# Performance work log

Hardware: AMD Instinct MI355X
Metric: run time of the kernel (lower is better)

## Reference

```python
import jax, jax.numpy as jnp
import numpy as np

TAU = 2.0      # LIF membrane time constant
VTH = 1.0      # firing threshold
ALPHA = 4.0    # sigmoid surrogate sharpness (spikingjelly default)
EPS = 1e-5     # BatchNorm eps


@jax.custom_vjp
def spike(x):
    # Heaviside forward, sigmoid surrogate backward
    return (x >= 0.0).astype(x.dtype)

def _spike_fwd(x):
    return (x >= 0.0).astype(x.dtype), x

def _spike_bwd(x, g):
    s = jax.nn.sigmoid(ALPHA * x)
    return (g * ALPHA * s * (1.0 - s),)

spike.defvjp(_spike_fwd, _spike_bwd)


def setup_inputs() -> dict:
    key = jax.random.key(0)
    k1, k2 = jax.random.split(key)
    T, B, C_in, C_out, M = 8, 16, 256, 256, 1024
    x = jax.random.normal(k1, (T, B, C_in, M), dtype=jnp.float32)
    W = jax.random.normal(k2, (C_out, C_in), dtype=jnp.float32) * 0.05  # 1x1 conv weight
    gamma = jnp.ones((C_out,), dtype=jnp.float32)
    beta = jnp.zeros((C_out,), dtype=jnp.float32)
    return {"x": x, "W": W, "gamma": gamma, "beta": beta}


def reference(x, W, gamma, beta):
    # 1x1 Conv1d over flattened (T*B) batch == channel contraction
    y = jnp.einsum('oc,tbcm->tbom', W, x)  # [T,B,C_out,M]
    # BatchNorm1d (training forward): per-channel stats over (T*B, M)
    mean = y.mean(axis=(0, 1, 3), keepdims=True)
    var = y.var(axis=(0, 1, 3), keepdims=True)
    y = (y - mean) * jax.lax.rsqrt(var + EPS)
    y = y * gamma[None, None, :, None] + beta[None, None, :, None]

    # Multi-step LIF: v <- v + (x - v)/tau; fire; hard reset to 0 (detached)
    def step(v, xt):
        v = v + (xt - v) / TAU
        s = spike(v - VTH)
        v = v * (1.0 - jax.lax.stop_gradient(s))
        return v, s

    v0 = jnp.zeros_like(y[0])
    _, spikes = jax.lax.scan(step, v0, y)
    return spikes  # [T,B,C_out,M]
```

## Files before the change

kernel.cpp:

```cpp
#include <hip/hip_runtime.h>

#define TT 8
#define BB 16
#define CC 256
#define MM 1024
#define NY 33554432


__device__ __forceinline__ float np_pairwise_1024(
    const float* __restrict__ yrow, float* __restrict__ scratch, int tid)
{
    if (tid < 64) {
        const int blk = tid >> 3;
        const int k   = tid & 7;
        const float* p = yrow + blk * 128 + k;
        float r = p[0];
#pragma unroll
        for (int i = 1; i < 16; ++i) r = __fadd_rn(r, p[8 * i]);
        scratch[tid] = r;
    }
    __syncthreads();
    if (tid == 0) {
        float B[8];
#pragma unroll
        for (int blk = 0; blk < 8; ++blk) {
            const float* r = scratch + blk * 8;
            const float s01 = __fadd_rn(r[0], r[1]);
            const float s23 = __fadd_rn(r[2], r[3]);
            const float s45 = __fadd_rn(r[4], r[5]);
            const float s67 = __fadd_rn(r[6], r[7]);
            B[blk] = __fadd_rn(__fadd_rn(s01, s23), __fadd_rn(s45, s67));
        }
        const float c0 = __fadd_rn(B[0], B[1]);
        const float c1 = __fadd_rn(B[2], B[3]);
        const float c2 = __fadd_rn(B[4], B[5]);
        const float c3 = __fadd_rn(B[6], B[7]);
        scratch[64] = __fadd_rn(__fadd_rn(c0, c1), __fadd_rn(c2, c3));
    }
    __syncthreads();
    return scratch[64];
}

__global__ __launch_bounds__(256) void einsum_store(
    const float* __restrict__ x, const float* __restrict__ W,
    float* __restrict__ y)
{
    __shared__ float wt[CC][8];
    const int tid = threadIdx.x;
    const int lin = blockIdx.x;
    const int xcd = lin & 7;
    const int j   = lin >> 3;
    const int og  = j & 31;
    const int tb  = xcd * 16 + (j >> 5);
    const int m0  = tid * 4;

#pragma unroll
    for (int i = 0; i < 8; ++i)
        wt[tid][i] = W[(size_t)(og * 8 + i) * CC + tid];
    __syncthreads();

    const float* xs = x + (size_t)tb * (CC * MM) + m0;

    float a[8][4];
#pragma unroll
    for (int i = 0; i < 8; ++i)
#pragma unroll
        for (int q = 0; q < 4; ++q) a[i][q] = 0.0f;

    for (int c = 0; c < CC; ++c) {
        const float4 xv = *(const float4*)(xs + (size_t)c * MM);
        const float4 w0 = *(const float4*)&wt[c][0];
        const float4 w1 = *(const float4*)&wt[c][4];
        const float wv[8] = {w0.x, w0.y, w0.z, w0.w, w1.x, w1.y, w1.z, w1.w};
#pragma unroll
        for (int i = 0; i < 8; ++i) {
            a[i][0] = __fadd_rn(a[i][0], __fmul_rn(wv[i], xv.x));
            a[i][1] = __fadd_rn(a[i][1], __fmul_rn(wv[i], xv.y));
            a[i][2] = __fadd_rn(a[i][2], __fmul_rn(wv[i], xv.z));
            a[i][3] = __fadd_rn(a[i][3], __fmul_rn(wv[i], xv.w));
        }
    }

#pragma unroll
    for (int i = 0; i < 8; ++i) {
        const int o = og * 8 + i;
        *(float4*)(y + ((size_t)tb * CC + o) * MM + m0) =
            make_float4(a[i][0], a[i][1], a[i][2], a[i][3]);
    }
}

__global__ __launch_bounds__(256) void mean_partial_y(
    const float* __restrict__ y, float* __restrict__ part)
{
    __shared__ float yrow[1024];
    __shared__ float scratch[65];
    const int tid = threadIdx.x;
    const int o  = blockIdx.x;
    const int tb = blockIdx.y;
    const int m0 = tid * 4;

    *(float4*)&yrow[m0] = *(const float4*)(y + ((size_t)tb * CC + o) * MM + m0);
    __syncthreads();
    const float P = np_pairwise_1024(yrow, scratch, tid);
    if (tid == 0) part[(size_t)tb * 256 + o] = P;
}

__global__ void reduce_mean(const float* __restrict__ part,
                            float* __restrict__ mv)
{
    const int o = threadIdx.x;
    float S = 0.0f;
    for (int tb = 0; tb < 128; ++tb)
        S = __fadd_rn(S, part[(size_t)tb * 256 + o]);
    mv[o] = S * (1.0f / 131072.0f);
}

__global__ __launch_bounds__(256) void var_partial_y(
    const float* __restrict__ y, const float* __restrict__ mv,
    float* __restrict__ part)
{
    __shared__ float yrow[1024];
    __shared__ float scratch[65];
    const int tid = threadIdx.x;
    const int o  = blockIdx.x;
    const int tb = blockIdx.y;
    const int m0 = tid * 4;

    const float mean = mv[o];
    const float4 yv = *(const float4*)(y + ((size_t)tb * CC + o) * MM + m0);
    const float d0 = __fsub_rn(yv.x, mean);
    const float d1 = __fsub_rn(yv.y, mean);
    const float d2 = __fsub_rn(yv.z, mean);
    const float d3 = __fsub_rn(yv.w, mean);
    *(float4*)&yrow[m0] = make_float4(__fmul_rn(d0, d0), __fmul_rn(d1, d1),
                                      __fmul_rn(d2, d2), __fmul_rn(d3, d3));
    __syncthreads();
    const float P = np_pairwise_1024(yrow, scratch, tid);
    if (tid == 0) part[(size_t)tb * 256 + o] = P;
}

__global__ void reduce_var(const float* __restrict__ part,
                           float* __restrict__ mv)
{
    const int o = threadIdx.x;
    float S = 0.0f;
    for (int tb = 0; tb < 128; ++tb)
        S = __fadd_rn(S, part[(size_t)tb * 256 + o]);
    const float var = S * (1.0f / 131072.0f);
    const float vp  = __fadd_rn(var, 1e-5f);
    mv[256 + o] = __fdiv_rn(1.0f, __fsqrt_rn(vp));
}

__global__ __launch_bounds__(256) void lif_from_y(
    const float* __restrict__ y, const float* __restrict__ mv,
    const float* __restrict__ gamma, const float* __restrict__ beta,
    float* __restrict__ out)
{
    const int tid = threadIdx.x;
    const int o = blockIdx.x;
    const int b = blockIdx.y;
    const int m0 = tid * 4;

    const float mean = mv[o];
    const float rs   = mv[256 + o];
    const float g    = gamma[o];
    const float be   = beta[o];

    float v0 = 0.0f, v1 = 0.0f, v2 = 0.0f, v3 = 0.0f;

    for (int t = 0; t < TT; ++t) {
        const size_t off = ((size_t)(t * BB + b) * CC + o) * MM + m0;
        const float4 yv = *(const float4*)(y + off);

        const float n0 = __fadd_rn(__fmul_rn(__fmul_rn(__fsub_rn(yv.x, mean), rs), g), be);
        const float n1 = __fadd_rn(__fmul_rn(__fmul_rn(__fsub_rn(yv.y, mean), rs), g), be);
        const float n2 = __fadd_rn(__fmul_rn(__fmul_rn(__fsub_rn(yv.z, mean), rs), g), be);
        const float n3 = __fadd_rn(__fmul_rn(__fmul_rn(__fsub_rn(yv.w, mean), rs), g), be);

        v0 = __fadd_rn(v0, __fmul_rn(__fsub_rn(n0, v0), 0.5f));
        v1 = __fadd_rn(v1, __fmul_rn(__fsub_rn(n1, v1), 0.5f));
        v2 = __fadd_rn(v2, __fmul_rn(__fsub_rn(n2, v2), 0.5f));
        v3 = __fadd_rn(v3, __fmul_rn(__fsub_rn(n3, v3), 0.5f));

        const bool s0 = (v0 >= 1.0f);
        const bool s1 = (v1 >= 1.0f);
        const bool s2 = (v2 >= 1.0f);
        const bool s3 = (v3 >= 1.0f);
        if (s0) v0 = 0.0f;
        if (s1) v1 = 0.0f;
        if (s2) v2 = 0.0f;
        if (s3) v3 = 0.0f;

        *(float4*)(out + off) = make_float4(s0 ? 1.0f : 0.0f, s1 ? 1.0f : 0.0f,
                                            s2 ? 1.0f : 0.0f, s3 ? 1.0f : 0.0f);
    }
}

__device__ __forceinline__ void e1_row4(
    const float* __restrict__ x, const float* __restrict__ W,
    int t, int b, int o, int m0,
    float& y0, float& y1, float& y2, float& y3)
{
    const float* xs = x + ((size_t)(t * BB + b) * CC) * MM + m0;
    const float* wr = W + (size_t)o * CC;
    y0 = 0.0f; y1 = 0.0f; y2 = 0.0f; y3 = 0.0f;
    for (int c = 0; c < CC; ++c) {
        const float wc = wr[c];
        const float4 xv = *(const float4*)(xs + (size_t)c * MM);
        y0 = __fadd_rn(y0, __fmul_rn(wc, xv.x));
        y1 = __fadd_rn(y1, __fmul_rn(wc, xv.y));
        y2 = __fadd_rn(y2, __fmul_rn(wc, xv.z));
        y3 = __fadd_rn(y3, __fmul_rn(wc, xv.w));
    }
}

__global__ __launch_bounds__(256) void pass_mean_fb(
    const float* __restrict__ x, const float* __restrict__ W,
    float* __restrict__ part)
{
    __shared__ float yrow[1024];
    __shared__ float scratch[65];
    const int tid = threadIdx.x;
    const int o  = blockIdx.x;
    const int tb = blockIdx.y;
    const int m0 = tid * 4;
    float y0, y1, y2, y3;
    e1_row4(x, W, tb >> 4, tb & 15, o, m0, y0, y1, y2, y3);
    *(float4*)&yrow[m0] = make_float4(y0, y1, y2, y3);
    __syncthreads();
    const float P = np_pairwise_1024(yrow, scratch, tid);
    if (tid == 0) part[(size_t)tb * 256 + o] = P;
}

__global__ __launch_bounds__(256) void pass_var_fb(
    const float* __restrict__ x, const float* __restrict__ W,
    const float* __restrict__ mv, float* __restrict__ part)
{
    __shared__ float yrow[1024];
    __shared__ float scratch[65];
    const int tid = threadIdx.x;
    const int o  = blockIdx.x;
    const int tb = blockIdx.y;
    const int m0 = tid * 4;
    const float mean = mv[o];
    float y0, y1, y2, y3;
    e1_row4(x, W, tb >> 4, tb & 15, o, m0, y0, y1, y2, y3);
    const float d0 = __fsub_rn(y0, mean);
    const float d1 = __fsub_rn(y1, mean);
    const float d2 = __fsub_rn(y2, mean);
    const float d3 = __fsub_rn(y3, mean);
    *(float4*)&yrow[m0] = make_float4(__fmul_rn(d0, d0), __fmul_rn(d1, d1),
                                      __fmul_rn(d2, d2), __fmul_rn(d3, d3));
    __syncthreads();
    const float P = np_pairwise_1024(yrow, scratch, tid);
    if (tid == 0) part[(size_t)tb * 256 + o] = P;
}

__global__ __launch_bounds__(256) void pass_lif_fb(
    const float* __restrict__ x, const float* __restrict__ W,
    const float* __restrict__ mv,
    const float* __restrict__ gamma, const float* __restrict__ beta,
    float* __restrict__ out)
{
    const int tid = threadIdx.x;
    const int o = blockIdx.x;
    const int b = blockIdx.y;
    const int m0 = tid * 4;
    const float mean = mv[o];
    const float rs   = mv[256 + o];
    const float g    = gamma[o];
    const float be   = beta[o];
    float v0 = 0.0f, v1 = 0.0f, v2 = 0.0f, v3 = 0.0f;
    for (int t = 0; t < TT; ++t) {
        float y0, y1, y2, y3;
        e1_row4(x, W, t, b, o, m0, y0, y1, y2, y3);
        const float n0 = __fadd_rn(__fmul_rn(__fmul_rn(__fsub_rn(y0, mean), rs), g), be);
        const float n1 = __fadd_rn(__fmul_rn(__fmul_rn(__fsub_rn(y1, mean), rs), g), be);
        const float n2 = __fadd_rn(__fmul_rn(__fmul_rn(__fsub_rn(y2, mean), rs), g), be);
        const float n3 = __fadd_rn(__fmul_rn(__fmul_rn(__fsub_rn(y3, mean), rs), g), be);
        v0 = __fadd_rn(v0, __fmul_rn(__fsub_rn(n0, v0), 0.5f));
        v1 = __fadd_rn(v1, __fmul_rn(__fsub_rn(n1, v1), 0.5f));
        v2 = __fadd_rn(v2, __fmul_rn(__fsub_rn(n2, v2), 0.5f));
        v3 = __fadd_rn(v3, __fmul_rn(__fsub_rn(n3, v3), 0.5f));
        const bool s0 = (v0 >= 1.0f);
        const bool s1 = (v1 >= 1.0f);
        const bool s2 = (v2 >= 1.0f);
        const bool s3 = (v3 >= 1.0f);
        if (s0) v0 = 0.0f;
        if (s1) v1 = 0.0f;
        if (s2) v2 = 0.0f;
        if (s3) v3 = 0.0f;
        const size_t off = ((size_t)(t * BB + b) * CC + o) * MM + m0;
        *(float4*)(out + off) = make_float4(s0 ? 1.0f : 0.0f, s1 ? 1.0f : 0.0f,
                                            s2 ? 1.0f : 0.0f, s3 ? 1.0f : 0.0f);
    }
}

extern "C" void kernel_launch(void* const* d_in, const int* in_sizes, int n_in,
                              void* d_out, int out_size, void* d_ws, size_t ws_size,
                              hipStream_t stream)
{
    const float* x     = (const float*)d_in[0];
    const float* W     = (const float*)d_in[1];
    const float* gamma = (const float*)d_in[2];
    const float* beta  = (const float*)d_in[3];
    float* out = (float*)d_out;

    const size_t need = ((size_t)NY + 128 * 256 + 512) * sizeof(float);

    if (ws_size >= need) {
        float* y    = (float*)d_ws;
        float* part = y + NY;
        float* mv   = part + 128 * 256;

        einsum_store<<<dim3(4096), dim3(256), 0, stream>>>(x, W, y);
        mean_partial_y<<<dim3(256, 128), dim3(256), 0, stream>>>(y, part);
        reduce_mean<<<dim3(1), dim3(256), 0, stream>>>(part, mv);
        var_partial_y<<<dim3(256, 128), dim3(256), 0, stream>>>(y, mv, part);
        reduce_var<<<dim3(1), dim3(256), 0, stream>>>(part, mv);
        lif_from_y<<<dim3(256, 16), dim3(256), 0, stream>>>(y, mv, gamma, beta, out);
    } else {
        float* part = (float*)d_ws;
        float* mv   = part + 128 * 256;
        pass_mean_fb<<<dim3(256, 128), dim3(256), 0, stream>>>(x, W, part);
        reduce_mean<<<dim3(1), dim3(256), 0, stream>>>(part, mv);
        pass_var_fb<<<dim3(256, 128), dim3(256), 0, stream>>>(x, W, mv, part);
        reduce_var<<<dim3(1), dim3(256), 0, stream>>>(part, mv);
        pass_lif_fb<<<dim3(256, 16), dim3(256), 0, stream>>>(x, W, mv, gamma, beta, out);
    }
}
```

Baseline: 506.6 us.

## Widen einsum output tile, prefetch x, and batch four rows per stats block

The einsum kernel now computes 16 output channels per block instead of 8, which halves the number of x re-reads across channel groups. It also software-prefetches the next four channel rows of x into registers while computing the current ones. The mean and variance partial kernels now reduce four rows per block, one wavefront per row, instead of one row per 256-thread block where most threads sat idle during the reduction. Costs are higher register pressure from 64 accumulators plus prefetch buffers, which may lower occupancy, and four times the shared memory in the stats kernels.

```diff
diff --git a/kernel.cpp b/kernel.cpp
--- a/kernel.cpp
+++ b/kernel.cpp
@@ -7,102 +7,123 @@
 #define NY 33554432
 
 
-__device__ __forceinline__ float np_pairwise_1024(
-    const float* __restrict__ yrow, float* __restrict__ scratch, int tid)
-{
-    if (tid < 64) {
-        const int blk = tid >> 3;
-        const int k   = tid & 7;
-        const float* p = yrow + blk * 128 + k;
+__global__ __launch_bounds__(256) void einsum_store(
+    const float* __restrict__ x, const float* __restrict__ W,
+    float* __restrict__ y)
+{
+    __shared__ float wt[CC][16];
+    const int tid = threadIdx.x;
+    const int lin = blockIdx.x;
+    const int xcd = lin & 7;
+    const int j   = lin >> 3;
+    const int og  = j & 15;
+    const int tb  = xcd * 16 + (j >> 4);
+    const int m0  = tid * 4;
+
+#pragma unroll
+    for (int i = 0; i < 16; ++i)
+        wt[tid][i] = W[(size_t)(og * 16 + i) * CC + tid];
+    __syncthreads();
+
+    const float* xs = x + (size_t)tb * (CC * MM) + m0;
+
+    float a[16][4];
+#pragma unroll
+    for (int i = 0; i < 16; ++i)
+#pragma unroll
+        for (int q = 0; q < 4; ++q) a[i][q] = 0.0f;
+
+    float4 xb[4];
+#pragma unroll
+    for (int q = 0; q < 4; ++q)
+        xb[q] = *(const float4*)(xs + (size_t)q * MM);
+
+    for (int cb = 0; cb < CC; cb += 4) {
+        float4 xn[4];
+        const bool more = (cb + 4 < CC);
+        if (more) {
+#pragma unroll
+            for (int q = 0; q < 4; ++q)
+                xn[q] = *(const float4*)(xs + (size_t)(cb + 4 + q) * MM);
+        }
+#pragma unroll
+        for (int q = 0; q < 4; ++q) {
+            const int c = cb + q;
+            const float4 w0 = *(const float4*)&wt[c][0];
+            const float4 w1 = *(const float4*)&wt[c][4];
+            const float4 w2 = *(const float4*)&wt[c][8];
+            const float4 w3 = *(const float4*)&wt[c][12];
+            const float wv[16] = {w0.x, w0.y, w0.z, w0.w,
+                                  w1.x, w1.y, w1.z, w1.w,
+                                  w2.x, w2.y, w2.z, w2.w,
+                                  w3.x, w3.y, w3.z, w3.w};
+#pragma unroll
+            for (int i = 0; i < 16; ++i) {
+                a[i][0] = __fadd_rn(a[i][0], __fmul_rn(wv[i], xb[q].x));
+                a[i][1] = __fadd_rn(a[i][1], __fmul_rn(wv[i], xb[q].y));
+                a[i][2] = __fadd_rn(a[i][2], __fmul_rn(wv[i], xb[q].z));
+                a[i][3] = __fadd_rn(a[i][3], __fmul_rn(wv[i], xb[q].w));
+            }
+        }
+        if (more) {
+#pragma unroll
+            for (int q = 0; q < 4; ++q) xb[q] = xn[q];
+        }
+    }
+
+#pragma unroll
+    for (int i = 0; i < 16; ++i) {
+        const int o = og * 16 + i;
+        *(float4*)(y + ((size_t)tb * CC + o) * MM + m0) =
+            make_float4(a[i][0], a[i][1], a[i][2], a[i][3]);
+    }
+}
+
+__global__ __launch_bounds__(256) void mean_partial_y(
+    const float* __restrict__ y, float* __restrict__ part)
+{
+    __shared__ float yrow[4][1024];
+    __shared__ float scratch[4][64];
+    const int tid  = threadIdx.x;
+    const int g    = tid >> 6;
+    const int lane = tid & 63;
+    const size_t row = (size_t)blockIdx.x * 4 + g;
+    const float* yr = y + row * MM;
+
+#pragma unroll
+    for (int q = 0; q < 4; ++q)
+        *(float4*)&yrow[g][q * 256 + lane * 4] =
+            *(const float4*)(yr + q * 256 + lane * 4);
+    __syncthreads();
+
+    {
+        const int blk = lane >> 3;
+        const int k   = lane & 7;
+        const float* p = &yrow[g][blk * 128 + k];
         float r = p[0];
 #pragma unroll
         for (int i = 1; i < 16; ++i) r = __fadd_rn(r, p[8 * i]);
-        scratch[tid] = r;
-    }
-    __syncthreads();
-    if (tid == 0) {
+        scratch[g][lane] = r;
+    }
+    __syncthreads();
+
+    if (lane == 0) {
         float B[8];
 #pragma unroll
-        for (int blk = 0; blk < 8; ++blk) {
-            const float* r = scratch + blk * 8;
+        for (int b2 = 0; b2 < 8; ++b2) {
+            const float* r = &scratch[g][b2 * 8];
             const float s01 = __fadd_rn(r[0], r[1]);
             const float s23 = __fadd_rn(r[2], r[3]);
             const float s45 = __fadd_rn(r[4], r[5]);
             const float s67 = __fadd_rn(r[6], r[7]);
-            B[blk] = __fadd_rn(__fadd_rn(s01, s23), __fadd_rn(s45, s67));
+            B[b2] = __fadd_rn(__fadd_rn(s01, s23), __fadd_rn(s45, s67));
         }
         const float c0 = __fadd_rn(B[0], B[1]);
         const float c1 = __fadd_rn(B[2], B[3]);
         const float c2 = __fadd_rn(B[4], B[5]);
         const float c3 = __fadd_rn(B[6], B[7]);
-        scratch[64] = __fadd_rn(__fadd_rn(c0, c1), __fadd_rn(c2, c3));
-    }
-    __syncthreads();
-    return scratch[64];
-}
-
-__global__ __launch_bounds__(256) void einsum_store(
-    const float* __restrict__ x, const float* __restrict__ W,
-    float* __restrict__ y)
-{
-    __shared__ float wt[CC][8];
-    const int tid = threadIdx.x;
-    const int lin = blockIdx.x;
-    const int xcd = lin & 7;
-    const int j   = lin >> 3;
-    const int og  = j & 31;
-    const int tb  = xcd * 16 + (j >> 5);
-    const int m0  = tid * 4;
-
-#pragma unroll
-    for (int i = 0; i < 8; ++i)
-        wt[tid][i] = W[(size_t)(og * 8 + i) * CC + tid];
-    __syncthreads();
-
-    const float* xs = x + (size_t)tb * (CC * MM) + m0;
-
-    float a[8][4];
-#pragma unroll
-    for (int i = 0; i < 8; ++i)
-#pragma unroll
-        for (int q = 0; q < 4; ++q) a[i][q] = 0.0f;
-
-    for (int c = 0; c < CC; ++c) {
-        const float4 xv = *(const float4*)(xs + (size_t)c * MM);
-        const float4 w0 = *(const float4*)&wt[c][0];
-        const float4 w1 = *(const float4*)&wt[c][4];
-        const float wv[8] = {w0.x, w0.y, w0.z, w0.w, w1.x, w1.y, w1.z, w1.w};
-#pragma unroll
-        for (int i = 0; i < 8; ++i) {
-            a[i][0] = __fadd_rn(a[i][0], __fmul_rn(wv[i], xv.x));
-            a[i][1] = __fadd_rn(a[i][1], __fmul_rn(wv[i], xv.y));
-            a[i][2] = __fadd_rn(a[i][2], __fmul_rn(wv[i], xv.z));
-            a[i][3] = __fadd_rn(a[i][3], __fmul_rn(wv[i], xv.w));
-        }
-    }
-
-#pragma unroll
-    for (int i = 0; i < 8; ++i) {
-        const int o = og * 8 + i;
-        *(float4*)(y + ((size_t)tb * CC + o) * MM + m0) =
-            make_float4(a[i][0], a[i][1], a[i][2], a[i][3]);
-    }
-}
-
-__global__ __launch_bounds__(256) void mean_partial_y(
-    const float* __restrict__ y, float* __restrict__ part)
-{
-    __shared__ float yrow[1024];
-    __shared__ float scratch[65];
-    const int tid = threadIdx.x;
-    const int o  = blockIdx.x;
-    const int tb = blockIdx.y;
-    const int m0 = tid * 4;
-
-    *(float4*)&yrow[m0] = *(const float4*)(y + ((size_t)tb * CC + o) * MM + m0);
-    __syncthreads();
-    const float P = np_pairwise_1024(yrow, scratch, tid);
-    if (tid == 0) part[(size_t)tb * 256 + o] = P;
+        part[row] = __fadd_rn(__fadd_rn(c0, c1), __fadd_rn(c2, c3));
+    }
 }
 
 __global__ void reduce_mean(const float* __restrict__ part,
@@ -119,24 +140,56 @@
     const float* __restrict__ y, const float* __restrict__ mv,
     float* __restrict__ part)
 {
-    __shared__ float yrow[1024];
-    __shared__ float scratch[65];
-    const int tid = threadIdx.x;
-    const int o  = blockIdx.x;
-    const int tb = blockIdx.y;
-    const int m0 = tid * 4;
-
-    const float mean = mv[o];
-    const float4 yv = *(const float4*)(y + ((size_t)tb * CC + o) * MM + m0);
-    const float d0 = __fsub_rn(yv.x, mean);
-    const float d1 = __fsub_rn(yv.y, mean);
-    const float d2 = __fsub_rn(yv.z, mean);
-    const float d3 = __fsub_rn(yv.w, mean);
-    *(float4*)&yrow[m0] = make_float4(__fmul_rn(d0, d0), __fmul_rn(d1, d1),
-                                      __fmul_rn(d2, d2), __fmul_rn(d3, d3));
-    __syncthreads();
-    const float P = np_pairwise_1024(yrow, scratch, tid);
-    if (tid == 0) part[(size_t)tb * 256 + o] = P;
+    __shared__ float yrow[4][1024];
+    __shared__ float scratch[4][64];
+    const int tid  = threadIdx.x;
+    const int g    = tid >> 6;
+    const int lane = tid & 63;
+    const size_t row = (size_t)blockIdx.x * 4 + g;
+    const float* yr = y + row * MM;
+    const float mean = mv[row & 255];
+
+#pragma unroll
+    for (int q = 0; q < 4; ++q) {
+        const float4 yv = *(const float4*)(yr + q * 256 + lane * 4);
+        const float d0 = __fsub_rn(yv.x, mean);
+        const float d1 = __fsub_rn(yv.y, mean);
+        const float d2 = __fsub_rn(yv.z, mean);
+        const float d3 = __fsub_rn(yv.w, mean);
+        *(float4*)&yrow[g][q * 256 + lane * 4] =
+            make_float4(__fmul_rn(d0, d0), __fmul_rn(d1, d1),
+                        __fmul_rn(d2, d2), __fmul_rn(d3, d3));
+    }
+    __syncthreads();
+
+    {
+        const int blk = lane >> 3;
+        const int k   = lane & 7;
+        const float* p = &yrow[g][blk * 128 + k];
+        float r = p[0];
+#pragma unroll
+        for (int i = 1; i < 16; ++i) r = __fadd_rn(r, p[8 * i]);
+        scratch[g][lane] = r;
+    }
+    __syncthreads();
+
+    if (lane == 0) {
+        float B[8];
+#pragma unroll
+        for (int b2 = 0; b2 < 8; ++b2) {
+            const float* r = &scratch[g][b2 * 8];
+            const float s01 = __fadd_rn(r[0], r[1]);
+            const float s23 = __fadd_rn(r[2], r[3]);
+            const float s45 = __fadd_rn(r[4], r[5]);
+            const float s67 = __fadd_rn(r[6], r[7]);
+            B[b2] = __fadd_rn(__fadd_rn(s01, s23), __fadd_rn(s45, s67));
+        }
+        const float c0 = __fadd_rn(B[0], B[1]);
+        const float c1 = __fadd_rn(B[2], B[3]);
+        const float c2 = __fadd_rn(B[4], B[5]);
+        const float c3 = __fadd_rn(B[6], B[7]);
+        part[row] = __fadd_rn(__fadd_rn(c0, c1), __fadd_rn(c2, c3));
+    }
 }
 
 __global__ void reduce_var(const float* __restrict__ part,
@@ -212,6 +265,40 @@
         y2 = __fadd_rn(y2, __fmul_rn(wc, xv.z));
         y3 = __fadd_rn(y3, __fmul_rn(wc, xv.w));
     }
+}
+
+__device__ __forceinline__ float np_pairwise_1024(
+    const float* __restrict__ yrow, float* __restrict__ scratch, int tid)
+{
+    if (tid < 64) {
+        const int blk = tid >> 3;
+        const int k   = tid & 7;
+        const float* p = yrow + blk * 128 + k;
+        float r = p[0];
+#pragma unroll
+        for (int i = 1; i < 16; ++i) r = __fadd_rn(r, p[8 * i]);
+        scratch[tid] = r;
+    }
+    __syncthreads();
+    if (tid == 0) {
+        float B[8];
+#pragma unroll
+        for (int blk = 0; blk < 8; ++blk) {
+            const float* r = scratch + blk * 8;
+            const float s01 = __fadd_rn(r[0], r[1]);
+            const float s23 = __fadd_rn(r[2], r[3]);
+            const float s45 = __fadd_rn(r[4], r[5]);
+            const float s67 = __fadd_rn(r[6], r[7]);
+            B[blk] = __fadd_rn(__fadd_rn(s01, s23), __fadd_rn(s45, s67));
+        }
+        const float c0 = __fadd_rn(B[0], B[1]);
+        const float c1 = __fadd_rn(B[2], B[3]);
+        const float c2 = __fadd_rn(B[4], B[5]);
+        const float c3 = __fadd_rn(B[6], B[7]);
+        scratch[64] = __fadd_rn(__fadd_rn(c0, c1), __fadd_rn(c2, c3));
+    }
+    __syncthreads();
+    return scratch[64];
 }
 
 __global__ __launch_bounds__(256) void pass_mean_fb(
@@ -313,10 +400,10 @@
         float* part = y + NY;
         float* mv   = part + 128 * 256;
 
-        einsum_store<<<dim3(4096), dim3(256), 0, stream>>>(x, W, y);
-        mean_partial_y<<<dim3(256, 128), dim3(256), 0, stream>>>(y, part);
+        einsum_store<<<dim3(2048), dim3(256), 0, stream>>>(x, W, y);
+        mean_partial_y<<<dim3(8192), dim3(256), 0, stream>>>(y, part);
         reduce_mean<<<dim3(1), dim3(256), 0, stream>>>(part, mv);
-        var_partial_y<<<dim3(256, 128), dim3(256), 0, stream>>>(y, mv, part);
+        var_partial_y<<<dim3(8192), dim3(256), 0, stream>>>(y, mv, part);
         reduce_var<<<dim3(1), dim3(256), 0, stream>>>(part, mv);
         lif_from_y<<<dim3(256, 16), dim3(256), 0, stream>>>(y, mv, gamma, beta, out);
     } else {
```

Result: faster. 478.8 us (-5.5%).
